# Optimization experiments

Hardware: AMD Instinct MI355X
Metric: run time of the kernel (lower is better)

The kernel has to match this reference:

```python
import jax, jax.numpy as jnp
import numpy as np

B, S, H = 2, 1024, 1024
NH, NKV, D = 8, 2, 128
ROT = 64                 # head_dim * partial_rotary_factor
E, K, NG, TG = 64, 8, 8, 4
FI, FSH = 512, 512       # moe_intermediate, shared intermediate (n_shared=1)
CAP = 512
EPS = 1e-5
SCALE = D ** -0.5
RSF = 1.0                # routed_scaling_factor
THETA = 10000.0


def rmsnorm(x, w):
    v = jnp.mean(x * x, axis=-1, keepdims=True)
    return x * jax.lax.rsqrt(v + EPS) * w


def rope(x, pos_f):
    # neox-style partial rotary: rotate first ROT dims of D, pass the rest
    half = ROT // 2
    inv = 1.0 / (THETA ** (jnp.arange(0, ROT, 2, dtype=jnp.float32) / ROT))
    ang = pos_f[:, None] * inv[None, :]                  # [S, half]
    cos = jnp.cos(ang)[None, :, None, :]                 # [1,S,1,half]
    sin = jnp.sin(ang)[None, :, None, :]
    x1, x2 = x[..., :half], x[..., half:ROT]
    return jnp.concatenate([x1 * cos - x2 * sin, x2 * cos + x1 * sin, x[..., ROT:]], axis=-1)


def setup_inputs() -> dict:
    ks = jax.random.split(jax.random.key(0), 16)
    s = 0.02
    return {
        'x': jax.random.normal(ks[0], (B, S, H), jnp.float32),
        'positions': jnp.arange(S, dtype=jnp.int32),
        'ln1_w': jnp.ones((H,), jnp.float32),
        'ln2_w': jnp.ones((H,), jnp.float32),
        'wqkv': jax.random.normal(ks[1], ((NH + 2 * NKV) * D, H), jnp.float32) * s,
        'bqkv': jax.random.normal(ks[2], ((NH + 2 * NKV) * D,), jnp.float32) * s,
        'qn_w': jnp.ones((D,), jnp.float32),
        'kn_w': jnp.ones((D,), jnp.float32),
        'wo': jax.random.normal(ks[3], (H, NH * D), jnp.float32) * s,
        'gate_w': jax.random.normal(ks[4], (E, H), jnp.float32) * s,
        'gate_b': jax.random.normal(ks[5], (E,), jnp.float32) * s,
        'w_gu': jax.random.normal(ks[6], (E, H, 2 * FI), jnp.float32) * s,
        'w_dn': jax.random.normal(ks[7], (E, FI, H), jnp.float32) * s,
        'sw_gu': jax.random.normal(ks[8], (H, 2 * FSH), jnp.float32) * s,
        'sw_dn': jax.random.normal(ks[9], (FSH, H), jnp.float32) * s,
    }


def _forward(x, positions, ln1_w, ln2_w, wqkv, bqkv, qn_w, kn_w, wo,
             gate_w, gate_b, w_gu, w_dn, sw_gu, sw_dn):
    # ---- attention block ----
    res = x
    h = rmsnorm(x, ln1_w)
    qkv = h @ wqkv.T + bqkv                               # [B,S,(NH+2NKV)*D]
    q, k, v = jnp.split(qkv, [NH * D, (NH + NKV) * D], axis=-1)
    q = q.reshape(B, S, NH, D)
    k = k.reshape(B, S, NKV, D)
    v = v.reshape(B, S, NKV, D)
    q = rmsnorm(q, qn_w)                                  # per-head qk-norm before rope
    k = rmsnorm(k, kn_w)
    pos_f = positions.astype(jnp.float32)
    q = rope(q, pos_f)
    k = rope(k, pos_f)
    kr = jnp.repeat(k, NH // NKV, axis=2)                 # GQA expand
    vr = jnp.repeat(v, NH // NKV, axis=2)
    scores = jnp.einsum('bqhd,bkhd->bhqk', q, kr) * SCALE
    causal = positions[:, None] >= positions[None, :]     # [S,S]
    scores = jnp.where(causal[None, None], scores, -jnp.inf)
    attn = jax.nn.softmax(scores, axis=-1)
    out = jnp.einsum('bhqk,bkhd->bqhd', attn, vr).reshape(B, S, NH * D)
    h = res + out @ wo.T

    # ---- MoE block ----
    res2 = h
    xt = rmsnorm(h, ln2_w).reshape(-1, H)                 # [T,H]
    T = xt.shape[0]
    logits = xt @ gate_w.T                                # [T,E]
    sc = jax.nn.sigmoid(logits)
    corr = sc + gate_b                                    # e_score_correction_bias
    # grouped top-k: score each group by sum of its top-2 corrected scores
    grp = jnp.sum(jax.lax.top_k(corr.reshape(T, NG, E // NG), 2)[0], axis=-1)  # [T,NG]
    gidx = jax.lax.top_k(grp, TG)[1]                      # [T,TG]
    gmask = jnp.sum(jax.nn.one_hot(gidx, NG, dtype=corr.dtype), axis=1)        # [T,NG]
    emask = jnp.repeat(gmask, E // NG, axis=1)            # [T,E]
    masked = jnp.where(emask > 0, corr, -jnp.inf)
    _, topi = jax.lax.top_k(masked, K)                    # [T,K]
    w = jnp.take_along_axis(sc, topi, axis=1)             # weights from raw sigmoid scores
    w = w / jnp.sum(w, axis=-1, keepdims=True) * RSF      # renormalize + scale

    # capacity-based dispatch -> grouped expert GEMM -> combine
    fe = topi.reshape(-1)                                 # [T*K]
    fw = w.reshape(-1)
    tid = jnp.repeat(jnp.arange(T), K)
    oh = (fe[:, None] == jnp.arange(E)[None, :]).astype(jnp.int32)
    pos_e = jnp.sum(jnp.cumsum(oh, axis=0) * oh, axis=-1) - 1                  # rank within expert
    valid = pos_e < CAP
    pos_safe = jnp.where(valid, pos_e, CAP)               # OOB scatter index -> dropped
    buf = jnp.zeros((E, CAP, H), xt.dtype).at[fe, pos_safe].set(xt[tid])
    gu = jnp.einsum('ech,ehf->ecf', buf, w_gu)            # [E,CAP,2FI]
    act = jax.nn.silu(gu[..., :FI]) * gu[..., FI:]
    eo = jnp.einsum('ecf,efh->ech', act, w_dn)            # [E,CAP,H]
    gathered = eo[fe, jnp.minimum(pos_safe, CAP - 1)] * (fw * valid)[:, None]
    routed = jax.ops.segment_sum(gathered, tid, num_segments=T)

    sgu = xt @ sw_gu                                      # shared expert (dense)
    shared = (jax.nn.silu(sgu[:, :FSH]) * sgu[:, FSH:]) @ sw_dn

    return res2 + (routed + shared).reshape(B, S, H)


def reference(x, positions, ln1_w, ln2_w, wqkv, bqkv, qn_w, kn_w, wo,
              gate_w, gate_b, w_gu, w_dn, sw_gu, sw_dn):
    return _forward(x, positions, ln1_w, ln2_w, wqkv, bqkv, qn_w, kn_w, wo,
                    gate_w, gate_b, w_gu, w_dn, sw_gu, sw_dn)
```

## Files before the change

### kernel.cpp

```cpp
#include <hip/hip_runtime.h>
#include <math.h>

#define S_LEN 1024
#define B_SZ 2
#define H_DIM 1024
#define NHQ 8
#define NKV 2
#define D_HEAD 128
#define NE 64
#define TOPK 8
#define NGRP 8
#define TGRP 4
#define FI_DIM 512
#define CAP 512
#define EPS_F 1e-5f
#define T_TOK (B_SZ * S_LEN)
#define QKV_DIM ((NHQ + 2 * NKV) * D_HEAD)
#define SCALE_F 0.08838834764831845f

typedef __attribute__((ext_vector_type(8))) short short8;
typedef __attribute__((ext_vector_type(4))) float floatx4;

__device__ inline short f2bf(float f) {
  union { float f; unsigned u; } v; v.f = f;
  unsigned r = (v.u + 0x7FFFu + ((v.u >> 16) & 1u)) >> 16;
  return (short)(r & 0xFFFFu);
}
__device__ inline float bf2f(short s) {
  union { unsigned u; float f; } v; v.u = ((unsigned)(unsigned short)s) << 16;
  return v.f;
}

__global__ __launch_bounds__(256) void rmsnorm_row(const float* __restrict__ x,
                                                   const float* __restrict__ w,
                                                   float* __restrict__ outf,
                                                   short* __restrict__ outb) {
  int t = blockIdx.x;
  int tid = threadIdx.x;
  const float* xp = x + (size_t)t * H_DIM;
  float4 v = *(const float4*)(xp + tid * 4);
  float ss = v.x * v.x + v.y * v.y + v.z * v.z + v.w * v.w;
  for (int i = 1; i < 64; i <<= 1) ss += __shfl_xor(ss, i);
  __shared__ float red[4];
  if ((tid & 63) == 0) red[tid >> 6] = ss;
  __syncthreads();
  float tot = red[0] + red[1] + red[2] + red[3];
  float rs = rsqrtf(tot / (float)H_DIM + EPS_F);
  float4 wv = *(const float4*)(w + tid * 4);
  float4 o;
  o.x = v.x * rs * wv.x; o.y = v.y * rs * wv.y;
  o.z = v.z * rs * wv.z; o.w = v.w * rs * wv.w;
  if (outf) *(float4*)(outf + (size_t)t * H_DIM + tid * 4) = o;
  short* bp = outb + (size_t)t * H_DIM + tid * 4;
  bp[0] = f2bf(o.x); bp[1] = f2bf(o.y); bp[2] = f2bf(o.z); bp[3] = f2bf(o.w);
}

__global__ __launch_bounds__(256) void gemm_nt_mfma(const short* __restrict__ A,
                                                    const float* __restrict__ W,
                                                    const float* __restrict__ bias,
                                                    const float* __restrict__ res,
                                                    float* __restrict__ C,
                                                    int M, int N, int K) {
  __shared__ __align__(16) short As[128 * 72];
  __shared__ __align__(16) short Bs[128 * 72];
  int tid = threadIdx.x;
  int m0 = blockIdx.y * 128, n0 = blockIdx.x * 128;
  int lane = tid & 63, wid = tid >> 6;
  int wm = (wid & 1) * 64, wn = (wid >> 1) * 64;
  floatx4 acc[4][4] = {};
  for (int k0 = 0; k0 < K; k0 += 64) {
    __syncthreads();
#pragma unroll
    for (int i = 0; i < 4; ++i) {
      int idx = tid + i * 256;
      int m = idx >> 3, c = idx & 7;
      *(int4*)(As + m * 72 + c * 8) = *(const int4*)(A + (size_t)(m0 + m) * K + k0 + c * 8);
    }
#pragma unroll
    for (int i = 0; i < 4; ++i) {
      int idx = tid + i * 256;
      int n = idx >> 3, c = idx & 7;
      const float* wp = W + (size_t)(n0 + n) * K + k0 + c * 8;
      float4 v0 = *(const float4*)(wp);
      float4 v1 = *(const float4*)(wp + 4);
      short8 b;
      b[0] = f2bf(v0.x); b[1] = f2bf(v0.y); b[2] = f2bf(v0.z); b[3] = f2bf(v0.w);
      b[4] = f2bf(v1.x); b[5] = f2bf(v1.y); b[6] = f2bf(v1.z); b[7] = f2bf(v1.w);
      *(short8*)(Bs + n * 72 + c * 8) = b;
    }
    __syncthreads();
#pragma unroll
    for (int ks = 0; ks < 2; ++ks) {
      int ko = ks * 32 + (lane >> 4) * 8;
      short8 af[4], bfg[4];
#pragma unroll
      for (int t = 0; t < 4; ++t)
        af[t] = *(const short8*)(As + (wm + t * 16 + (lane & 15)) * 72 + ko);
#pragma unroll
      for (int t = 0; t < 4; ++t)
        bfg[t] = *(const short8*)(Bs + (wn + t * 16 + (lane & 15)) * 72 + ko);
#pragma unroll
      for (int mt = 0; mt < 4; ++mt)
#pragma unroll
        for (int nt = 0; nt < 4; ++nt)
          acc[mt][nt] = __builtin_amdgcn_mfma_f32_16x16x32_bf16(af[mt], bfg[nt], acc[mt][nt], 0, 0, 0);
    }
  }
  int q = lane >> 4, cl = lane & 15;
#pragma unroll
  for (int mt = 0; mt < 4; ++mt)
#pragma unroll
    for (int nt = 0; nt < 4; ++nt)
#pragma unroll
      for (int r = 0; r < 4; ++r) {
        int m = m0 + wm + mt * 16 + q * 4 + r;
        int n = n0 + wn + nt * 16 + cl;
        float v = acc[mt][nt][r];
        if (bias) v += bias[n];
        if (res) v += res[(size_t)m * N + n];
        C[(size_t)m * N + n] = v;
      }
}

__global__ __launch_bounds__(64) void qknorm_rope(const float* __restrict__ qkv,
                                                  const int* __restrict__ positions,
                                                  const float* __restrict__ qn_w,
                                                  const float* __restrict__ kn_w,
                                                  short* __restrict__ qbo,
                                                  short* __restrict__ kbo,
                                                  short* __restrict__ vtbo) {
  int t = blockIdx.x;
  int head = blockIdx.y;
  int lane = threadIdx.x;
  int b = t >> 10;
  int s = t & (S_LEN - 1);
  if (head >= NHQ + NKV) {
    int kvh = head - (NHQ + NKV);
    const float* vp = qkv + (size_t)t * QKV_DIM + (NHQ + NKV) * D_HEAD + kvh * D_HEAD;
    short* vt = vtbo + (size_t)(b * NKV + kvh) * D_HEAD * S_LEN + s;
    vt[(size_t)lane * S_LEN] = f2bf(vp[lane]);
    vt[(size_t)(lane + 64) * S_LEN] = f2bf(vp[lane + 64]);
    return;
  }
  bool isq = head < NHQ;
  int off = isq ? head * D_HEAD : (NHQ * D_HEAD + (head - NHQ) * D_HEAD);
  const float* ptr = qkv + (size_t)t * QKV_DIM + off;
  const float* w = isq ? qn_w : kn_w;
  float x0 = ptr[lane];
  float x1 = ptr[lane + 64];
  float ss = x0 * x0 + x1 * x1;
  for (int i = 1; i < 64; i <<= 1) ss += __shfl_xor(ss, i);
  float rs = rsqrtf(ss / (float)D_HEAD + EPS_F);
  x0 = x0 * rs * w[lane];
  x1 = x1 * rs * w[lane + 64];
  float pos = (float)positions[s];
  int i2 = lane & 31;
  float invf = powf(10000.0f, -(float)i2 / 32.0f);
  float ang = pos * invf;
  float c = cosf(ang), sn = sinf(ang);
  float other = __shfl_xor(x0, 32);
  float r = (lane < 32) ? (x0 * c - other * sn) : (x0 * c + other * sn);
  if (isq) {
    short* qo = qbo + ((size_t)(b * NHQ + head) * S_LEN + s) * D_HEAD;
    qo[lane] = f2bf(r * SCALE_F);
    qo[lane + 64] = f2bf(x1 * SCALE_F);
  } else {
    short* ko = kbo + ((size_t)(b * NKV + (head - NHQ)) * S_LEN + s) * D_HEAD;
    ko[lane] = f2bf(r);
    ko[lane + 64] = f2bf(x1);
  }
}

__global__ __launch_bounds__(256) void attn_mfma(const short* __restrict__ qb,
                                                 const short* __restrict__ kb,
                                                 const short* __restrict__ vtb,
                                                 short* __restrict__ attnout) {
  __shared__ __align__(16) short Pb[4][16 * 36];
  int tid = threadIdx.x;
  int lane = tid & 63, wid = tid >> 6;
  int l15 = lane & 15, l4 = lane >> 4;
  int bx = blockIdx.x;
  int bh = bx >> 4;
  int g = bx & 15;
  int qt = (wid == 0) ? g : (wid == 1) ? (31 - g) : (wid == 2) ? (32 + g) : (63 - g);
  int b = bh >> 3, h = bh & 7, kvh = h >> 2;
  int qb0 = qt * 16;
  short* Pw = Pb[wid];

  const short* qp = qb + ((size_t)(b * NHQ + h) * S_LEN + qb0 + l15) * D_HEAD + l4 * 8;
  short8 qf[4];
#pragma unroll
  for (int c = 0; c < 4; ++c) qf[c] = *(const short8*)(qp + c * 32);

  const short* kbp = kb + (size_t)(b * NKV + kvh) * S_LEN * D_HEAD;
  const short* vbp = vtb + (size_t)(b * NKV + kvh) * D_HEAD * S_LEN;

  float m[4] = {-1e30f, -1e30f, -1e30f, -1e30f};
  float l[4] = {0.f, 0.f, 0.f, 0.f};
  floatx4 o[8] = {};

  int nkt = qb0 / 32 + 1;
  for (int kt = 0; kt < nkt; ++kt) {
    int kb0 = kt * 32;
    const short* kp = kbp + (size_t)(kb0 + l15) * D_HEAD + l4 * 8;
    floatx4 s0 = {}, s1 = {};
#pragma unroll
    for (int c = 0; c < 4; ++c) {
      short8 k0 = *(const short8*)(kp + c * 32);
      short8 k1 = *(const short8*)(kp + 16 * D_HEAD + c * 32);
      s0 = __builtin_amdgcn_mfma_f32_16x16x32_bf16(qf[c], k0, s0, 0, 0, 0);
      s1 = __builtin_amdgcn_mfma_f32_16x16x32_bf16(qf[c], k1, s1, 0, 0, 0);
    }
    if (kt == nkt - 1) {
#pragma unroll
      for (int r = 0; r < 4; ++r) {
        int qrow = qb0 + l4 * 4 + r;
        if (kb0 + l15 > qrow) s0[r] = -1e30f;
        if (kb0 + 16 + l15 > qrow) s1[r] = -1e30f;
      }
    }
    float al[4];
#pragma unroll
    for (int r = 0; r < 4; ++r) {
      float tm = fmaxf(s0[r], s1[r]);
      tm = fmaxf(tm, __shfl_xor(tm, 1));
      tm = fmaxf(tm, __shfl_xor(tm, 2));
      tm = fmaxf(tm, __shfl_xor(tm, 4));
      tm = fmaxf(tm, __shfl_xor(tm, 8));
      float mn = fmaxf(m[r], tm);
      al[r] = __expf(m[r] - mn);
      m[r] = mn;
      float p0 = __expf(s0[r] - mn);
      float p1 = __expf(s1[r] - mn);
      s0[r] = p0; s1[r] = p1;
      float ts = p0 + p1;
      ts += __shfl_xor(ts, 1);
      ts += __shfl_xor(ts, 2);
      ts += __shfl_xor(ts, 4);
      ts += __shfl_xor(ts, 8);
      l[r] = l[r] * al[r] + ts;
    }
#pragma unroll
    for (int dt = 0; dt < 8; ++dt)
#pragma unroll
      for (int r = 0; r < 4; ++r) o[dt][r] *= al[r];
    __builtin_amdgcn_wave_barrier();
#pragma unroll
    for (int r = 0; r < 4; ++r) {
      int prow = l4 * 4 + r;
      Pw[prow * 36 + l15] = f2bf(s0[r]);
      Pw[prow * 36 + 16 + l15] = f2bf(s1[r]);
    }
    __builtin_amdgcn_wave_barrier();
    short4 pa0 = *(const short4*)(Pw + l15 * 36 + l4 * 8);
    short4 pa1 = *(const short4*)(Pw + l15 * 36 + l4 * 8 + 4);
    short8 pf;
    pf[0] = pa0.x; pf[1] = pa0.y; pf[2] = pa0.z; pf[3] = pa0.w;
    pf[4] = pa1.x; pf[5] = pa1.y; pf[6] = pa1.z; pf[7] = pa1.w;
#pragma unroll
    for (int dt = 0; dt < 8; ++dt) {
      short8 vf = *(const short8*)(vbp + (size_t)(dt * 16 + l15) * S_LEN + kb0 + l4 * 8);
      o[dt] = __builtin_amdgcn_mfma_f32_16x16x32_bf16(pf, vf, o[dt], 0, 0, 0);
    }
  }
  float inv[4];
#pragma unroll
  for (int r = 0; r < 4; ++r) inv[r] = 1.f / l[r];
#pragma unroll
  for (int dt = 0; dt < 8; ++dt)
#pragma unroll
    for (int r = 0; r < 4; ++r) {
      int qrow = qb0 + l4 * 4 + r;
      attnout[(size_t)(b * S_LEN + qrow) * (NHQ * D_HEAD) + h * D_HEAD + dt * 16 + l15] =
          f2bf(o[dt][r] * inv[r]);
    }
}

__global__ __launch_bounds__(64) void gating_kernel(const float* __restrict__ xt,
                                                    const float* __restrict__ gate_w,
                                                    const float* __restrict__ gate_b,
                                                    int* __restrict__ topi,
                                                    float* __restrict__ fw) {
  __shared__ float xs[H_DIM];
  __shared__ float sc[NE];
  __shared__ float corr[NE];
  __shared__ float grp[NGRP];
  int t = blockIdx.x;
  int e = threadIdx.x;
  for (int i = e; i < H_DIM; i += 64) xs[i] = xt[(size_t)t * H_DIM + i];
  __syncthreads();
  const float* gw = gate_w + (size_t)e * H_DIM;
  float acc = 0.f;
  for (int h = 0; h < H_DIM; ++h) acc = fmaf(xs[h], gw[h], acc);
  float s = 1.f / (1.f + expf(-acc));
  sc[e] = s;
  corr[e] = s + gate_b[e];
  __syncthreads();
  if (e < NGRP) {
    float m1 = -1e30f, m2 = -1e30f;
    for (int j = 0; j < NE / NGRP; ++j) {
      float v = corr[e * 8 + j];
      if (v > m1) { m2 = m1; m1 = v; }
      else if (v > m2) m2 = v;
    }
    grp[e] = m1 + m2;
  }
  __syncthreads();
  if (e == 0) {
    bool gsel[NGRP];
    for (int g = 0; g < NGRP; ++g) gsel[g] = false;
    for (int it = 0; it < TGRP; ++it) {
      int bi = -1; float bv = -1e30f;
      for (int g = 0; g < NGRP; ++g)
        if (!gsel[g] && grp[g] > bv) { bv = grp[g]; bi = g; }
      gsel[bi] = true;
    }
    bool ch[NE];
    for (int i2 = 0; i2 < NE; ++i2) ch[i2] = false;
    int sel[TOPK];
    float wsum = 0.f;
    for (int it = 0; it < TOPK; ++it) {
      int bi = -1; float bv = -1e30f;
      for (int x2 = 0; x2 < NE; ++x2) {
        if (!gsel[x2 >> 3] || ch[x2]) continue;
        if (corr[x2] > bv) { bv = corr[x2]; bi = x2; }
      }
      ch[bi] = true;
      sel[it] = bi;
      wsum += sc[bi];
    }
    float inv = 1.f / wsum;
    for (int it = 0; it < TOPK; ++it) {
      topi[t * TOPK + it] = sel[it];
      fw[t * TOPK + it] = sc[sel[it]] * inv;
    }
  }
}

__global__ __launch_bounds__(256) void scan_kernel(const int* __restrict__ topi,
                                                   int* __restrict__ perm,
                                                   int* __restrict__ ecnt) {
  __shared__ int hist[256 * 65];
  int tid = threadIdx.x;
  for (int i = tid; i < 256 * 65; i += 256) hist[i] = 0;
  __syncthreads();
  int loc[64];
#pragma unroll
  for (int j = 0; j < 64; j += 4) {
    int4 v = *(const int4*)(topi + tid * 64 + j);
    loc[j] = v.x; loc[j + 1] = v.y; loc[j + 2] = v.z; loc[j + 3] = v.w;
  }
#pragma unroll
  for (int j = 0; j < 64; ++j) hist[tid * 65 + loc[j]]++;
  __syncthreads();
  if (tid < 64) {
    int run = 0;
    for (int c = 0; c < 256; ++c) {
      int v = hist[c * 65 + tid];
      hist[c * 65 + tid] = run;
      run += v;
    }
    ecnt[tid] = run < CAP ? run : CAP;
  }
  __syncthreads();
#pragma unroll
  for (int j = 0; j < 64; ++j) {
    int e = loc[j];
    int pos = hist[tid * 65 + e]++;
    if (pos < CAP) perm[e * CAP + pos] = tid * 64 + j;
  }
}

__global__ void zero_kernel(float4* __restrict__ p) {
  p[(size_t)blockIdx.x * 256 + threadIdx.x] = make_float4(0.f, 0.f, 0.f, 0.f);
}

__global__ __launch_bounds__(256) void moe_gu_mfma(const short* __restrict__ xtb,
                                                   const float* __restrict__ w_gu,
                                                   const float* __restrict__ sw_gu,
                                                   const int* __restrict__ perm,
                                                   const int* __restrict__ ecnt,
                                                   short* __restrict__ actR,
                                                   short* __restrict__ actS) {
  __shared__ int tok[128];
  __shared__ __align__(16) short As[128 * 72];
  __shared__ __align__(16) short Bs[128 * 72];
  int tid = threadIdx.x;
  int bx = blockIdx.x;
  int lane = tid & 63, wid = tid >> 6;
  bool sh = bx >= 256;
  int e = 0, base, rows;
  const float* wg;
  short* actp;
  if (!sh) {
    e = bx >> 2; base = (bx & 3) * 128;
    int cnt = ecnt[e];
    if (base >= cnt) return;
    rows = cnt - base; if (rows > 128) rows = 128;
    wg = w_gu + (size_t)e * H_DIM * (2 * FI_DIM);
    actp = actR + (size_t)(e * CAP + base) * FI_DIM;
  } else {
    base = (bx - 256) * 128; rows = 128;
    wg = sw_gu;
    actp = actS + (size_t)base * FI_DIM;
  }
  if (tid < 128) {
    int m = tid < rows ? tid : (rows - 1);
    tok[tid] = sh ? (base + tid) : (perm[e * CAP + base + m] >> 3);
  }
  __syncthreads();
  int mh = (wid & 1) * 64;
  int uh = wid >> 1;
  for (int jc = 0; jc < 8; ++jc) {
    floatx4 acc[4][4] = {};
    for (int k0 = 0; k0 < H_DIM; k0 += 64) {
      __syncthreads();
#pragma unroll
      for (int i = 0; i < 4; ++i) {
        int idx = tid + i * 256;
        int m = idx >> 3, c = idx & 7;
        *(int4*)(As + m * 72 + c * 8) =
            *(const int4*)(xtb + (size_t)tok[m] * H_DIM + k0 + c * 8);
      }
#pragma unroll
      for (int i = 0; i < 4; ++i) {
        int idx = tid + i * 256;
        int kc = idx >> 7, n2 = idx & 127;
        int col = (n2 < 64) ? (jc * 64 + n2) : (FI_DIM + jc * 64 + (n2 - 64));
        const float* wp = wg + (size_t)(k0 + kc * 8) * (2 * FI_DIM) + col;
        short8 b;
#pragma unroll
        for (int j = 0; j < 8; ++j) b[j] = f2bf(wp[(size_t)j * (2 * FI_DIM)]);
        *(short8*)(Bs + n2 * 72 + kc * 8) = b;
      }
      __syncthreads();
#pragma unroll
      for (int ks = 0; ks < 2; ++ks) {
        int ko = ks * 32 + (lane >> 4) * 8;
        short8 af[4], bfg[4];
#pragma unroll
        for (int t = 0; t < 4; ++t)
          af[t] = *(const short8*)(As + (mh + t * 16 + (lane & 15)) * 72 + ko);
#pragma unroll
        for (int t = 0; t < 4; ++t)
          bfg[t] = *(const short8*)(Bs + (uh * 64 + t * 16 + (lane & 15)) * 72 + ko);
#pragma unroll
        for (int mt = 0; mt < 4; ++mt)
#pragma unroll
          for (int nt = 0; nt < 4; ++nt)
            acc[mt][nt] = __builtin_amdgcn_mfma_f32_16x16x32_bf16(af[mt], bfg[nt], acc[mt][nt], 0, 0, 0);
      }
    }
    __syncthreads();
    int q = lane >> 4, cl = lane & 15;
    if (uh == 0) {
#pragma unroll
      for (int mt = 0; mt < 4; ++mt)
#pragma unroll
        for (int nt = 0; nt < 4; ++nt)
#pragma unroll
          for (int r = 0; r < 4; ++r) {
            int row = mh + mt * 16 + q * 4 + r;
            int col = nt * 16 + cl;
            Bs[row * 72 + col] = f2bf(acc[mt][nt][r]);
          }
    }
    __syncthreads();
    if (uh == 1) {
#pragma unroll
      for (int mt = 0; mt < 4; ++mt)
#pragma unroll
        for (int nt = 0; nt < 4; ++nt)
#pragma unroll
          for (int r = 0; r < 4; ++r) {
            int row = mh + mt * 16 + q * 4 + r;
            int col = nt * 16 + cl;
            float g = bf2f(Bs[row * 72 + col]);
            float u = acc[mt][nt][r];
            float a = g / (1.f + expf(-g)) * u;
            actp[(size_t)row * FI_DIM + jc * 64 + col] = f2bf(a);
          }
    }
  }
}

__global__ __launch_bounds__(256) void moe_dn_mfma(const short* __restrict__ actR,
                                                   const short* __restrict__ actS,
                                                   const float* __restrict__ w_dn,
                                                   const float* __restrict__ sw_dn,
                                                   const int* __restrict__ perm,
                                                   const int* __restrict__ ecnt,
                                                   const float* __restrict__ fw,
                                                   float* __restrict__ moe_acc) {
  __shared__ int tok[128];
  __shared__ float wts[128];
  __shared__ __align__(16) short As[128 * 72];
  __shared__ __align__(16) short Bs[128 * 72];
  int tid = threadIdx.x;
  int bx = blockIdx.x;
  int lane = tid & 63, wid = tid >> 6;
  bool sh = bx >= 256;
  int e = 0, base, rows;
  const float* wd;
  const short* actp;
  if (!sh) {
    e = bx >> 2; base = (bx & 3) * 128;
    int cnt = ecnt[e];
    if (base >= cnt) return;
    rows = cnt - base; if (rows > 128) rows = 128;
    wd = w_dn + (size_t)e * FI_DIM * H_DIM;
    actp = actR + (size_t)(e * CAP + base) * FI_DIM;
  } else {
    base = (bx - 256) * 128; rows = 128;
    wd = sw_dn;
    actp = actS + (size_t)base * FI_DIM;
  }
  if (tid < 128) {
    if (sh) { tok[tid] = base + tid; wts[tid] = 1.f; }
    else if (tid < rows) {
      int pi = perm[e * CAP + base + tid];
      tok[tid] = pi >> 3;
      wts[tid] = fw[pi];
    } else { tok[tid] = 0; wts[tid] = 0.f; }
  }
  __syncthreads();
  int mh = (wid & 1) * 64, wn = (wid >> 1) * 64;
  for (int jc = 0; jc < 8; ++jc) {
    floatx4 acc[4][4] = {};
    for (int k0 = 0; k0 < FI_DIM; k0 += 64) {
      __syncthreads();
#pragma unroll
      for (int i = 0; i < 4; ++i) {
        int idx = tid + i * 256;
        int m = idx >> 3, c = idx & 7;
        *(int4*)(As + m * 72 + c * 8) =
            *(const int4*)(actp + (size_t)m * FI_DIM + k0 + c * 8);
      }
#pragma unroll
      for (int i = 0; i < 4; ++i) {
        int idx = tid + i * 256;
        int kc = idx >> 7, n2 = idx & 127;
        const float* wp = wd + (size_t)(k0 + kc * 8) * H_DIM + jc * 128 + n2;
        short8 b;
#pragma unroll
        for (int j = 0; j < 8; ++j) b[j] = f2bf(wp[(size_t)j * H_DIM]);
        *(short8*)(Bs + n2 * 72 + kc * 8) = b;
      }
      __syncthreads();
#pragma unroll
      for (int ks = 0; ks < 2; ++ks) {
        int ko = ks * 32 + (lane >> 4) * 8;
        short8 af[4], bfg[4];
#pragma unroll
        for (int t = 0; t < 4; ++t)
          af[t] = *(const short8*)(As + (mh + t * 16 + (lane & 15)) * 72 + ko);
#pragma unroll
        for (int t = 0; t < 4; ++t)
          bfg[t] = *(const short8*)(Bs + (wn + t * 16 + (lane & 15)) * 72 + ko);
#pragma unroll
        for (int mt = 0; mt < 4; ++mt)
#pragma unroll
          for (int nt = 0; nt < 4; ++nt)
            acc[mt][nt] = __builtin_amdgcn_mfma_f32_16x16x32_bf16(af[mt], bfg[nt], acc[mt][nt], 0, 0, 0);
      }
    }
    __syncthreads();
    int q = lane >> 4, cl = lane & 15;
#pragma unroll
    for (int mt = 0; mt < 4; ++mt)
#pragma unroll
      for (int nt = 0; nt < 4; ++nt)
#pragma unroll
        for (int r = 0; r < 4; ++r) {
          int row = mh + mt * 16 + q * 4 + r;
          if (row < rows) {
            int col = jc * 128 + wn + nt * 16 + cl;
            unsafeAtomicAdd(moe_acc + (size_t)tok[row] * H_DIM + col,
                            acc[mt][nt][r] * wts[row]);
          }
        }
  }
}

__global__ void combine_kernel(const float4* __restrict__ a, const float4* __restrict__ b,
                               float4* __restrict__ o) {
  size_t i = (size_t)blockIdx.x * 256 + threadIdx.x;
  float4 x = a[i], y = b[i];
  o[i] = make_float4(x.x + y.x, x.y + y.y, x.z + y.z, x.w + y.w);
}

extern "C" void kernel_launch(void* const* d_in, const int* in_sizes, int n_in,
                              void* d_out, int out_size, void* d_ws, size_t ws_size,
                              hipStream_t stream) {
  const float* x = (const float*)d_in[0];
  const int* positions = (const int*)d_in[1];
  const float* ln1_w = (const float*)d_in[2];
  const float* ln2_w = (const float*)d_in[3];
  const float* wqkv = (const float*)d_in[4];
  const float* bqkv = (const float*)d_in[5];
  const float* qn_w = (const float*)d_in[6];
  const float* kn_w = (const float*)d_in[7];
  const float* wo = (const float*)d_in[8];
  const float* gate_w = (const float*)d_in[9];
  const float* gate_b = (const float*)d_in[10];
  const float* w_gu = (const float*)d_in[11];
  const float* w_dn = (const float*)d_in[12];
  const float* sw_gu = (const float*)d_in[13];
  const float* sw_dn = (const float*)d_in[14];
  float* out = (float*)d_out;

  float* p = (float*)d_ws;
  float* h2 = p;        p += 2097152;
  float* xt = p;        p += 2097152;
  short* xtb = (short*)p; p += 1048576;
  float* moe_acc = p;   p += 2097152;
  float* fw = p;        p += 16384;
  int* topi = (int*)p;  p += 16384;
  int* perm = (int*)p;  p += 32768;
  int* ecnt = (int*)p;  p += 64;
  float* pool = p;
  short* h1b = (short*)pool;
  float* qkv = pool + 1048576;
  short* attnb = (short*)(pool + 4194304);
  short* qb_s  = (short*)(pool + 5242880);
  short* kb_s  = (short*)(pool + 6291456);
  short* vtb_s = (short*)(pool + 6553600);
  short* actR = (short*)pool;
  short* actS = (short*)(pool + 8388608);

  rmsnorm_row<<<T_TOK, 256, 0, stream>>>(x, ln1_w, nullptr, h1b);
  gemm_nt_mfma<<<dim3(QKV_DIM / 128, T_TOK / 128), 256, 0, stream>>>(
      h1b, wqkv, bqkv, nullptr, qkv, T_TOK, QKV_DIM, H_DIM);
  qknorm_rope<<<dim3(T_TOK, NHQ + 2 * NKV), 64, 0, stream>>>(qkv, positions, qn_w, kn_w,
                                                             qb_s, kb_s, vtb_s);
  attn_mfma<<<256, 256, 0, stream>>>(qb_s, kb_s, vtb_s, attnb);
  gemm_nt_mfma<<<dim3(H_DIM / 128, T_TOK / 128), 256, 0, stream>>>(
      attnb, wo, nullptr, x, h2, T_TOK, H_DIM, NHQ * D_HEAD);
  rmsnorm_row<<<T_TOK, 256, 0, stream>>>(h2, ln2_w, xt, xtb);
  gating_kernel<<<T_TOK, 64, 0, stream>>>(xt, gate_w, gate_b, topi, fw);
  zero_kernel<<<2048, 256, 0, stream>>>((float4*)moe_acc);
  scan_kernel<<<1, 256, 0, stream>>>(topi, perm, ecnt);
  moe_gu_mfma<<<256 + T_TOK / 128, 256, 0, stream>>>(xtb, w_gu, sw_gu, perm, ecnt, actR, actS);
  moe_dn_mfma<<<256 + T_TOK / 128, 256, 0, stream>>>(actR, actS, w_dn, sw_dn, perm, ecnt, fw, moe_acc);
  combine_kernel<<<2048, 256, 0, stream>>>((const float4*)h2, (const float4*)moe_acc, (float4*)out);
}
```

Measured before the change: 1.740 ms.

## Batch 16 tokens per gating block and read a transposed gate weight

The gating kernel now handles 16 tokens per 256-thread block. Each thread computes 4 token logits for one expert, reading weights from a gate matrix transposed once into the workspace by a new small kernel. This gives coalesced weight loads and reuses each weight load across 4 tokens, where the old version used one 64-thread block per token with strided per-thread weight reads. The cost is an extra transpose launch, 64KB+ of LDS per block (which limits occupancy), and 16 serial top-k threads per block.

```diff
diff --git a/kernel.cpp b/kernel.cpp
--- a/kernel.cpp
+++ b/kernel.cpp
@@ -276,43 +276,94 @@
     }
 }
 
-__global__ __launch_bounds__(64) void gating_kernel(const float* __restrict__ xt,
-                                                    const float* __restrict__ gate_w,
-                                                    const float* __restrict__ gate_b,
-                                                    int* __restrict__ topi,
-                                                    float* __restrict__ fw) {
-  __shared__ float xs[H_DIM];
-  __shared__ float sc[NE];
-  __shared__ float corr[NE];
-  __shared__ float grp[NGRP];
-  int t = blockIdx.x;
-  int e = threadIdx.x;
-  for (int i = e; i < H_DIM; i += 64) xs[i] = xt[(size_t)t * H_DIM + i];
-  __syncthreads();
-  const float* gw = gate_w + (size_t)e * H_DIM;
-  float acc = 0.f;
-  for (int h = 0; h < H_DIM; ++h) acc = fmaf(xs[h], gw[h], acc);
-  float s = 1.f / (1.f + expf(-acc));
-  sc[e] = s;
-  corr[e] = s + gate_b[e];
-  __syncthreads();
-  if (e < NGRP) {
+__global__ __launch_bounds__(256) void gate_transpose(const float* __restrict__ gw,
+                                                      float* __restrict__ gwT) {
+  __shared__ float tile[64][65];
+  int k0 = blockIdx.x * 64;
+  int tid = threadIdx.x;
+  for (int i = tid; i < 64 * 64; i += 256) {
+    int e = i >> 6, ki = i & 63;
+    tile[e][ki] = gw[(size_t)e * H_DIM + k0 + ki];
+  }
+  __syncthreads();
+  for (int i = tid; i < 64 * 64; i += 256) {
+    int ki = i >> 6, e = i & 63;
+    gwT[(size_t)(k0 + ki) * NE + e] = tile[e][ki];
+  }
+}
+
+__global__ __launch_bounds__(256) void gate_kernel(const float* __restrict__ xt,
+                                                   const float* __restrict__ gwT,
+                                                   const float* __restrict__ gate_b,
+                                                   int* __restrict__ topi,
+                                                   float* __restrict__ fw) {
+  __shared__ float xs[16][H_DIM];
+  __shared__ float scs[16][NE];
+  __shared__ float corrs[16][NE];
+  __shared__ float grps[16][NGRP];
+  int tid = threadIdx.x;
+  int t0 = blockIdx.x * 16;
+  for (int i = tid; i < 16 * 256; i += 256) {
+    int t = i >> 8, c = i & 255;
+    *(float4*)&xs[t][c * 4] = *(const float4*)(xt + (size_t)(t0 + t) * H_DIM + c * 4);
+  }
+  __syncthreads();
+  int e = tid & 63, tq = tid >> 6;
+  const float* x0 = xs[tq * 4 + 0];
+  const float* x1 = xs[tq * 4 + 1];
+  const float* x2 = xs[tq * 4 + 2];
+  const float* x3 = xs[tq * 4 + 3];
+  floatx4 a0 = {}, a1 = {}, a2 = {}, a3 = {};
+  for (int k = 0; k < H_DIM; k += 4) {
+    float w0 = gwT[(size_t)(k + 0) * NE + e];
+    float w1 = gwT[(size_t)(k + 1) * NE + e];
+    float w2 = gwT[(size_t)(k + 2) * NE + e];
+    float w3 = gwT[(size_t)(k + 3) * NE + e];
+    float4 v0 = *(const float4*)(x0 + k);
+    float4 v1 = *(const float4*)(x1 + k);
+    float4 v2 = *(const float4*)(x2 + k);
+    float4 v3 = *(const float4*)(x3 + k);
+    a0[0] = fmaf(v0.x, w0, a0[0]); a0[1] = fmaf(v0.y, w1, a0[1]);
+    a0[2] = fmaf(v0.z, w2, a0[2]); a0[3] = fmaf(v0.w, w3, a0[3]);
+    a1[0] = fmaf(v1.x, w0, a1[0]); a1[1] = fmaf(v1.y, w1, a1[1]);
+    a1[2] = fmaf(v1.z, w2, a1[2]); a1[3] = fmaf(v1.w, w3, a1[3]);
+    a2[0] = fmaf(v2.x, w0, a2[0]); a2[1] = fmaf(v2.y, w1, a2[1]);
+    a2[2] = fmaf(v2.z, w2, a2[2]); a2[3] = fmaf(v2.w, w3, a2[3]);
+    a3[0] = fmaf(v3.x, w0, a3[0]); a3[1] = fmaf(v3.y, w1, a3[1]);
+    a3[2] = fmaf(v3.z, w2, a3[2]); a3[3] = fmaf(v3.w, w3, a3[3]);
+  }
+  float b = gate_b[e];
+  float lg[4];
+  lg[0] = (a0[0] + a0[1]) + (a0[2] + a0[3]);
+  lg[1] = (a1[0] + a1[1]) + (a1[2] + a1[3]);
+  lg[2] = (a2[0] + a2[1]) + (a2[2] + a2[3]);
+  lg[3] = (a3[0] + a3[1]) + (a3[2] + a3[3]);
+#pragma unroll
+  for (int j = 0; j < 4; ++j) {
+    float s = 1.f / (1.f + expf(-lg[j]));
+    scs[tq * 4 + j][e] = s;
+    corrs[tq * 4 + j][e] = s + b;
+  }
+  __syncthreads();
+  if (tid < 128) {
+    int t = tid >> 3, g = tid & 7;
     float m1 = -1e30f, m2 = -1e30f;
     for (int j = 0; j < NE / NGRP; ++j) {
-      float v = corr[e * 8 + j];
+      float v = corrs[t][g * 8 + j];
       if (v > m1) { m2 = m1; m1 = v; }
       else if (v > m2) m2 = v;
     }
-    grp[e] = m1 + m2;
-  }
-  __syncthreads();
-  if (e == 0) {
+    grps[t][g] = m1 + m2;
+  }
+  __syncthreads();
+  if (tid < 16) {
+    int t = tid;
     bool gsel[NGRP];
     for (int g = 0; g < NGRP; ++g) gsel[g] = false;
     for (int it = 0; it < TGRP; ++it) {
       int bi = -1; float bv = -1e30f;
       for (int g = 0; g < NGRP; ++g)
-        if (!gsel[g] && grp[g] > bv) { bv = grp[g]; bi = g; }
+        if (!gsel[g] && grps[t][g] > bv) { bv = grps[t][g]; bi = g; }
       gsel[bi] = true;
     }
     bool ch[NE];
@@ -323,16 +374,17 @@
       int bi = -1; float bv = -1e30f;
       for (int x2 = 0; x2 < NE; ++x2) {
         if (!gsel[x2 >> 3] || ch[x2]) continue;
-        if (corr[x2] > bv) { bv = corr[x2]; bi = x2; }
+        if (corrs[t][x2] > bv) { bv = corrs[t][x2]; bi = x2; }
       }
       ch[bi] = true;
       sel[it] = bi;
-      wsum += sc[bi];
-    }
-    float inv = 1.f / wsum;
+      wsum += scs[t][bi];
+    }
+    float invw = 1.f / wsum;
+    int gt = t0 + t;
     for (int it = 0; it < TOPK; ++it) {
-      topi[t * TOPK + it] = sel[it];
-      fw[t * TOPK + it] = sc[sel[it]] * inv;
+      topi[gt * TOPK + it] = sel[it];
+      fw[gt * TOPK + it] = scs[t][sel[it]] * invw;
     }
   }
 }
@@ -618,6 +670,7 @@
   int* topi = (int*)p;  p += 16384;
   int* perm = (int*)p;  p += 32768;
   int* ecnt = (int*)p;  p += 64;
+  float* gwT = p;       p += 65536;
   float* pool = p;
   short* h1b = (short*)pool;
   float* qkv = pool + 1048576;
@@ -628,6 +681,7 @@
   short* actR = (short*)pool;
   short* actS = (short*)(pool + 8388608);
 
+  gate_transpose<<<16, 256, 0, stream>>>(gate_w, gwT);
   rmsnorm_row<<<T_TOK, 256, 0, stream>>>(x, ln1_w, nullptr, h1b);
   gemm_nt_mfma<<<dim3(QKV_DIM / 128, T_TOK / 128), 256, 0, stream>>>(
       h1b, wqkv, bqkv, nullptr, qkv, T_TOK, QKV_DIM, H_DIM);
@@ -637,7 +691,7 @@
   gemm_nt_mfma<<<dim3(H_DIM / 128, T_TOK / 128), 256, 0, stream>>>(
       attnb, wo, nullptr, x, h2, T_TOK, H_DIM, NHQ * D_HEAD);
   rmsnorm_row<<<T_TOK, 256, 0, stream>>>(h2, ln2_w, xt, xtb);
-  gating_kernel<<<T_TOK, 64, 0, stream>>>(xt, gate_w, gate_b, topi, fw);
+  gate_kernel<<<T_TOK / 16, 256, 0, stream>>>(xt, gwT, gate_b, topi, fw);
   zero_kernel<<<2048, 256, 0, stream>>>((float4*)moe_acc);
   scan_kernel<<<1, 256, 0, stream>>>(topi, perm, ecnt);
   moe_gu_mfma<<<256 + T_TOK / 128, 256, 0, stream>>>(xtb, w_gu, sw_gu, perm, ecnt, actR, actS);
```

New measurement: 1.563 ms. 10.2% less time.
